# Kernel tuning notes

Measured on AMD Instinct MI355X. Metric: run time of the kernel, lower is better.

## Reference

```python
import jax, jax.numpy as jnp
import numpy as np

B = 8192      # rows after reshape(-1, seq_len)
S = 512       # seq_len
H = 256       # d_model (GRU hidden size)
P = 96        # pred_len
IN = 1        # GRUCell input size (scalar per step)


def setup_inputs() -> dict:
    key = jax.random.key(0)
    ks = jax.random.split(key, 7)
    s = 1.0 / np.sqrt(H)  # torch GRUCell init scale
    return {
        "x": jax.random.normal(ks[0], (B, S), dtype=jnp.float32),
        "W_ih": jax.random.uniform(ks[1], (3 * H, IN), jnp.float32, -s, s),
        "W_hh": jax.random.uniform(ks[2], (3 * H, H), jnp.float32, -s, s),
        "b_ih": jax.random.uniform(ks[3], (3 * H,), jnp.float32, -s, s),
        "b_hh": jax.random.uniform(ks[4], (3 * H,), jnp.float32, -s, s),
        "W_out": jax.random.uniform(ks[5], (P, H), jnp.float32, -s, s),
        "b_out": jax.random.uniform(ks[6], (P,), jnp.float32, -s, s),
    }


def reference(x, W_ih, W_hh, b_ih, b_hh, W_out, b_out):
    # Precompute input-side gate pre-activations for all timesteps at once:
    # x: [B, S], W_ih: [3H, 1] -> gi: [S, B, 3H]
    gi = x.T[:, :, None] * W_ih[:, 0][None, None, :] + b_ih  # [S, B, 3H]

    def step(h, gi_t):
        gh = h @ W_hh.T + b_hh                 # [B, 3H]
        i_r, i_z, i_n = jnp.split(gi_t, 3, axis=-1)
        h_r, h_z, h_n = jnp.split(gh, 3, axis=-1)
        r = jax.nn.sigmoid(i_r + h_r)
        z = jax.nn.sigmoid(i_z + h_z)
        n = jnp.tanh(i_n + r * h_n)
        h_new = (1.0 - z) * n + z * h
        return h_new, None

    h0 = jnp.zeros((x.shape[0], H), dtype=x.dtype)
    h_final, _ = jax.lax.scan(step, h0, gi)
    out = h_final @ W_out.T + b_out            # [B, P]
    return out.reshape(-1, P, 1)
```

## Files before the change

### kernel.cpp

```cpp
#include <hip/hip_runtime.h>
#include <math.h>

#define B_ROWS 8192
#define S_LEN  512
#define H_DIM  256
#define G3     768
#define P_DIM  96
#define TB     32

typedef __attribute__((ext_vector_type(8))) _Float16 half8;
typedef __attribute__((ext_vector_type(4))) float floatx4;

__device__ __forceinline__ float sigmoid_fast(float v) {
    return 1.0f / (1.0f + __expf(-v));
}
__device__ __forceinline__ float tanh_fast(float v) {
    return 1.0f - 2.0f / (__expf(2.0f * v) + 1.0f);
}
__device__ __forceinline__ unsigned short f32_f16(float f) {
    _Float16 h = (_Float16)f;
    return __builtin_bit_cast(unsigned short, h);
}
__device__ __forceinline__ int rot3(int l) { return ((l << 3) | (l >> 3)) & 63; }

__global__ void pack_weights(const float* __restrict__ W_hh,
                             const float* __restrict__ W_out,
                             unsigned short* __restrict__ Bh,
                             unsigned short* __restrict__ Bl,
                             float* __restrict__ WoT,
                             unsigned int* __restrict__ ctr) {
    const int j = blockIdx.x;
    const int k = threadIdx.x;
    const float wv = W_hh[j * H_DIM + k];
    const unsigned short hi = f32_f16(wv);
    const float hf = (float)__builtin_bit_cast(_Float16, hi);
    const unsigned short lo = f32_f16(wv - hf);
    const int idx = (((k >> 5) * 48 + (j >> 4)) * 64 +
                     ((j & 15) | (((k >> 3) & 3) << 4))) * 8 + (k & 7);
    Bh[idx] = hi;
    Bl[idx] = lo;
    if (j < P_DIM) WoT[k * P_DIM + j] = W_out[j * H_DIM + k];
    if (j == 0 && k == 0) *ctr = 0u;
}

#define A_OFF   0
#define X_OFF   32768
#define W_OFF   36864
#define LDS_SZ  135168

__device__ __forceinline__ void mfma2(floatx4& c0, floatx4& c1,
                                      const half8& a0, const half8& a1,
                                      const half8& bh, const half8& bl) {
    c0 = __builtin_amdgcn_mfma_f32_16x16x32_f16(a0, bh, c0, 0, 0, 0);
    c1 = __builtin_amdgcn_mfma_f32_16x16x32_f16(a1, bh, c1, 0, 0, 0);
    c0 = __builtin_amdgcn_mfma_f32_16x16x32_f16(a0, bl, c0, 0, 0, 0);
    c1 = __builtin_amdgcn_mfma_f32_16x16x32_f16(a1, bl, c1, 0, 0, 0);
}

__device__ __forceinline__ void gissue1(half8 (&BH)[6],
                                        const unsigned short* (&pbh)[6],
                                        int kc) {
#pragma unroll
    for (int gh = 0; gh < 6; ++gh)
        BH[gh] = *(const half8*)(pbh[gh] + (size_t)kc * 24576);
}

__device__ __forceinline__ void ahread(half8 (&AH)[2], const char* Ac,
                                       int kc, int rl) {
#pragma unroll
    for (int mt = 0; mt < 2; ++mt)
        AH[mt] = *(const half8*)(Ac + (kc * 2 + mt) * 1024 + rl * 16);
}

__device__ __forceinline__ void kcmfma1(floatx4 (&acc)[3][2][2],
                                        const half8 (&AH)[2],
                                        const half8 (&BH)[6]) {
#pragma unroll
    for (int gh = 0; gh < 6; ++gh) {
        floatx4& c0 = acc[gh >> 1][0][gh & 1];
        floatx4& c1 = acc[gh >> 1][1][gh & 1];
        c0 = __builtin_amdgcn_mfma_f32_16x16x32_f16(AH[0], BH[gh], c0, 0, 0, 0);
        c1 = __builtin_amdgcn_mfma_f32_16x16x32_f16(AH[1], BH[gh], c1, 0, 0, 0);
    }
}

__device__ __forceinline__ void kcmfma(floatx4 (&acc)[3][2][2],
                                       const half8 (&AH)[2],
                                       const half8 (&BH)[6],
                                       const half8 (&BL)[6]) {
#pragma unroll
    for (int gh = 0; gh < 6; ++gh)
        mfma2(acc[gh >> 1][0][gh & 1], acc[gh >> 1][1][gh & 1],
              AH[0], AH[1], BH[gh], BL[gh]);
}

__global__ __launch_bounds__(512, 2)
void gru_mfma(const float* __restrict__ x,
              const float* __restrict__ W_ih,
              const float* __restrict__ b_ih,
              const float* __restrict__ b_hh,
              const unsigned short* __restrict__ Bh,
              const unsigned short* __restrict__ Bl,
              const float* __restrict__ WoT,
              const float* __restrict__ b_out,
              float* __restrict__ out,
              unsigned int* __restrict__ ctr) {
    __shared__ __align__(16) char smem[LDS_SZ];

    const int tid  = threadIdx.x;
    const int w    = tid >> 6;
    const int lane = tid & 63;
    const int q    = lane >> 4;
    const int c    = lane & 15;
    const int row0 = blockIdx.x * TB;

    float wih[3][2], bcc[2][2], bihn[2], bhhn[2];
#pragma unroll
    for (int g = 0; g < 3; ++g)
#pragma unroll
        for (int ht = 0; ht < 2; ++ht) {
            const int col = g * H_DIM + w * 32 + ht * 16 + c;
            wih[g][ht] = W_ih[col];
            if (g < 2) {
                bcc[g][ht] = b_ih[col] + b_hh[col];
            } else {
                bihn[ht] = b_ih[col];
                bhhn[ht] = b_hh[col];
            }
        }

    const unsigned short* pbh[6];
    const unsigned short* pbl[6];
#pragma unroll
    for (int gh = 0; gh < 6; ++gh) {
        const size_t toff = (size_t)((gh >> 1) * 16 + w * 2 + (gh & 1)) * 512 + lane * 8;
        pbh[gh] = Bh + toff;
        pbl[gh] = Bl + toff;
    }

    half8 r7h[6], r7l[6];
#pragma unroll
    for (int gh = 0; gh < 6; ++gh) {
        r7h[gh] = *(const half8*)(pbh[gh] + 7 * 24576);
        r7l[gh] = *(const half8*)(pbl[gh] + 7 * 24576);
    }

    for (int i = tid; i < 96 * 64; i += 512) {
        const int slot = i >> 6, l16 = i & 63;
        const unsigned short* src = (slot < 48)
            ? (Bh + (size_t)(288 + slot) * 512 + l16 * 8)
            : (Bl + (size_t)(288 + slot - 48) * 512 + l16 * 8);
        *(uint4*)(smem + W_OFF + slot * 1024 + l16 * 16) = *(const uint4*)src;
    }

    for (int i = tid; i < 8192; i += 512) ((int*)(smem + A_OFF))[i] = 0;
    float* xt = (float*)(smem + X_OFF);
    {
        const int r = tid >> 4, t2 = tid & 15;
        xt[r * 16 + t2] = x[(size_t)(row0 + r) * S_LEN + t2];
    }
    __syncthreads();

    float h_own[2][2][4];
#pragma unroll
    for (int mt = 0; mt < 2; ++mt)
#pragma unroll
        for (int ht = 0; ht < 2; ++ht)
#pragma unroll
            for (int r = 0; r < 4; ++r) h_own[mt][ht][r] = 0.0f;

    const int rl = rot3(lane);

    int soff[2][4];
#pragma unroll
    for (int ht = 0; ht < 2; ++ht)
#pragma unroll
        for (int r = 0; r < 4; ++r) {
            const int d = (q * 4 + r) | ((2 * ht + (c >> 3)) << 4);
            soff[ht][r] = rot3(d) * 16 + (c & 7) * 2;
        }
    int xbase[2][4];
#pragma unroll
    for (int mt = 0; mt < 2; ++mt)
#pragma unroll
        for (int r = 0; r < 4; ++r)
            xbase[mt][r] = (q * 4 + r + 16 * mt) * 16;
    const char* w6base[6];
#pragma unroll
    for (int gh = 0; gh < 6; ++gh) {
        const int T = (gh >> 1) * 16 + w * 2 + (gh & 1);
        w6base[gh] = smem + W_OFF + T * 1024 + lane * 16;
    }

    half8 b0h[6], b1h[6];
    half8 ahA[2], ahB[2];

    gissue1(b0h, pbh, 0);

#pragma unroll 1
    for (int t = 0; t < S_LEN; ++t) {
#pragma unroll
        for (int gh = 0; gh < 6; ++gh)
            asm volatile("" : "+v"(pbh[gh]));

        const int cur = t & 1, nxt = cur ^ 1;
        const char* Ac = smem + A_OFF + cur * 16384;

        ahread(ahA, Ac, 0, rl);
        gissue1(b1h, pbh, 1);

        const int xidx = ((t >> 4) & 1) * 512 + (t & 15);
        float xr[2][4];
#pragma unroll
        for (int mt = 0; mt < 2; ++mt)
#pragma unroll
            for (int r = 0; r < 4; ++r)
                xr[mt][r] = xt[xbase[mt][r] + xidx];

        floatx4 acc[3][2][2];
#pragma unroll
        for (int mt = 0; mt < 2; ++mt)
#pragma unroll
            for (int ht = 0; ht < 2; ++ht)
#pragma unroll
                for (int r = 0; r < 4; ++r) {
                    acc[0][mt][ht][r] = fmaf(xr[mt][r], wih[0][ht], bcc[0][ht]);
                    acc[1][mt][ht][r] = fmaf(xr[mt][r], wih[1][ht], bcc[1][ht]);
                    acc[2][mt][ht][r] = bhhn[ht];
                }

        ahread(ahB, Ac, 1, rl);
        kcmfma1(acc, ahA, b0h);
        gissue1(b0h, pbh, 2);
        ahread(ahA, Ac, 2, rl);
        kcmfma1(acc, ahB, b1h);
        gissue1(b1h, pbh, 3);
        ahread(ahB, Ac, 3, rl);
        kcmfma1(acc, ahA, b0h);
        gissue1(b0h, pbh, 4);
        ahread(ahA, Ac, 4, rl);
        kcmfma1(acc, ahB, b1h);
        gissue1(b1h, pbh, 5);
        ahread(ahB, Ac, 5, rl);
        kcmfma1(acc, ahA, b0h);
        ahread(ahA, Ac, 6, rl);
        kcmfma1(acc, ahB, b1h);

        {
            half8 w6h[6], w6l[6];
#pragma unroll
            for (int gh = 0; gh < 6; ++gh) {
                w6h[gh] = *(const half8*)(w6base[gh]);
                w6l[gh] = *(const half8*)(w6base[gh] + 48 * 1024);
            }
            ahread(ahB, Ac, 7, rl);
            kcmfma(acc, ahA, w6h, w6l);
        }

        gissue1(b0h, pbh, 0);
        kcmfma(acc, ahB, r7h, r7l);

        char* Anx = smem + A_OFF + nxt * 16384;
#pragma unroll
        for (int mt = 0; mt < 2; ++mt) {
            char* ch = Anx + (w * 2 + mt) * 1024;
#pragma unroll
            for (int ht = 0; ht < 2; ++ht)
#pragma unroll
                for (int r = 0; r < 4; ++r) {
                    const float rr  = sigmoid_fast(acc[0][mt][ht][r]);
                    const float zz  = sigmoid_fast(acc[1][mt][ht][r]);
                    const float inn = fmaf(xr[mt][r], wih[2][ht], bihn[ht]);
                    const float nn  = tanh_fast(fmaf(rr, acc[2][mt][ht][r], inn));
                    const float hv  = (1.0f - zz) * nn + zz * h_own[mt][ht][r];
                    h_own[mt][ht][r] = hv;
                    *(unsigned short*)(ch + soff[ht][r]) = f32_f16(hv);
                }
        }

        const bool tick = ((t & 15) == 15) && (t != S_LEN - 1);
        if (tick) {
            const int r = tid >> 4, t2 = tid & 15;
            xt[((((t + 1) >> 4) & 1) * 32 + r) * 16 + t2] =
                x[(size_t)(row0 + r) * S_LEN + (t + 1) + t2];
        }
        __syncthreads();

        if (tick) {
            if (tid == 0) {
                const unsigned int tgt = 256u * (unsigned)((t >> 4) + 1);
                atomicAdd(ctr, 1u);
                for (int spin = 0; spin < (1 << 17); ++spin) {
                    if (__hip_atomic_load(ctr, __ATOMIC_RELAXED,
                                          __HIP_MEMORY_SCOPE_AGENT) >= tgt) break;
                    __builtin_amdgcn_s_sleep(4);
                }
            }
            __syncthreads();
        }
    }

    float* hfin = (float*)(smem);
#pragma unroll
    for (int mt = 0; mt < 2; ++mt)
#pragma unroll
        for (int ht = 0; ht < 2; ++ht)
#pragma unroll
            for (int r = 0; r < 4; ++r) {
                const int m = q * 4 + r + 16 * mt;
                const int k = w * 32 + ht * 16 + c;
                hfin[m * H_DIM + k] = h_own[mt][ht][r];
            }
    __syncthreads();

    if (tid < 256) {
        const int cid   = tid & 63;
        const int rid   = tid >> 6;
        const int myrow = rid * 8;
        const int pA    = cid;
        const int pB    = 64 + cid;
        const bool hasB = (cid < 32);
        float accA[8], accB[8];
#pragma unroll
        for (int rr = 0; rr < 8; ++rr) { accA[rr] = 0.0f; accB[rr] = 0.0f; }

        for (int k = 0; k < H_DIM; k += 4) {
            float4 hv[8];
#pragma unroll
            for (int rr = 0; rr < 8; ++rr)
                hv[rr] = *(const float4*)&hfin[(myrow + rr) * H_DIM + k];
            float wA[4], wB[4];
#pragma unroll
            for (int kk = 0; kk < 4; ++kk) {
                wA[kk] = WoT[(size_t)(k + kk) * P_DIM + pA];
                wB[kk] = hasB ? WoT[(size_t)(k + kk) * P_DIM + pB] : 0.0f;
            }
#pragma unroll
            for (int kk = 0; kk < 4; ++kk)
#pragma unroll
                for (int rr = 0; rr < 8; ++rr) {
                    const float hvv = (&hv[rr].x)[kk];
                    accA[rr] = fmaf(hvv, wA[kk], accA[rr]);
                    accB[rr] = fmaf(hvv, wB[kk], accB[rr]);
                }
        }
        const float boA = b_out[pA];
        const float boB = hasB ? b_out[pB] : 0.0f;
#pragma unroll
        for (int rr = 0; rr < 8; ++rr) {
            const size_t orow = (size_t)(row0 + myrow + rr) * P_DIM;
            out[orow + pA] = accA[rr] + boA;
            if (hasB) out[orow + pB] = accB[rr] + boB;
        }
    }
}

__global__ __launch_bounds__(256, 1)
void gru_fallback(const float* __restrict__ x,
                  const float* __restrict__ W_ih,
                  const float* __restrict__ Whh,
                  const float* __restrict__ b_ih,
                  const float* __restrict__ b_hh,
                  const float* __restrict__ Wout,
                  const float* __restrict__ b_out,
                  float* __restrict__ out) {
    __shared__ float hbuf[2][TB][H_DIM];

    const int tid   = threadIdx.x;
    const int cid   = tid & 63;
    const int rid   = tid >> 6;
    const int row0  = blockIdx.x * TB;
    const int myrow = rid * 8;
    const int c0    = cid * 4;

    float wih[3][4], bc[2][4], bihn[4], bhhn[4];
#pragma unroll
    for (int cc = 0; cc < 4; ++cc) {
        const int j = c0 + cc;
        wih[0][cc] = W_ih[j];
        wih[1][cc] = W_ih[H_DIM + j];
        wih[2][cc] = W_ih[2 * H_DIM + j];
        bc[0][cc]  = b_ih[j] + b_hh[j];
        bc[1][cc]  = b_ih[H_DIM + j] + b_hh[H_DIM + j];
        bihn[cc]   = b_ih[2 * H_DIM + j];
        bhhn[cc]   = b_hh[2 * H_DIM + j];
    }
    for (int i = tid; i < TB * H_DIM; i += 256) (&hbuf[0][0][0])[i] = 0.0f;
    float h_own[8][4];
#pragma unroll
    for (int rr = 0; rr < 8; ++rr)
#pragma unroll
        for (int cc = 0; cc < 4; ++cc) h_own[rr][cc] = 0.0f;
    __syncthreads();

    int p = 0;
    for (int t = 0; t < S_LEN; ++t) {
        float xv[8];
#pragma unroll
        for (int rr = 0; rr < 8; ++rr)
            xv[rr] = x[(size_t)(row0 + myrow + rr) * S_LEN + t];

        float acc[3][8][4];
#pragma unroll
        for (int rr = 0; rr < 8; ++rr)
#pragma unroll
            for (int cc = 0; cc < 4; ++cc) {
                acc[0][rr][cc] = fmaf(xv[rr], wih[0][cc], bc[0][cc]);
                acc[1][rr][cc] = fmaf(xv[rr], wih[1][cc], bc[1][cc]);
                acc[2][rr][cc] = bhhn[cc];
            }
        const float* hb = &hbuf[p][0][0];
        for (int k = 0; k < H_DIM; k += 4) {
            float4 hv[8];
#pragma unroll
            for (int rr = 0; rr < 8; ++rr)
                hv[rr] = *(const float4*)(hb + (myrow + rr) * H_DIM + k);
#pragma unroll
            for (int g = 0; g < 3; ++g)
#pragma unroll
                for (int kk = 0; kk < 4; ++kk) {
                    float wrow[4];
#pragma unroll
                    for (int cc = 0; cc < 4; ++cc)
                        wrow[cc] = Whh[(size_t)(g * H_DIM + c0 + cc) * H_DIM + k + kk];
#pragma unroll
                    for (int rr = 0; rr < 8; ++rr) {
                        const float hvv = (&hv[rr].x)[kk];
#pragma unroll
                        for (int cc = 0; cc < 4; ++cc)
                            acc[g][rr][cc] = fmaf(hvv, wrow[cc], acc[g][rr][cc]);
                    }
                }
        }
#pragma unroll
        for (int rr = 0; rr < 8; ++rr) {
            float4 hnew;
#pragma unroll
            for (int cc = 0; cc < 4; ++cc) {
                const float r_  = sigmoid_fast(acc[0][rr][cc]);
                const float z_  = sigmoid_fast(acc[1][rr][cc]);
                const float i_n = fmaf(xv[rr], wih[2][cc], bihn[cc]);
                const float n_  = tanh_fast(fmaf(r_, acc[2][rr][cc], i_n));
                const float hv2 = (1.0f - z_) * n_ + z_ * h_own[rr][cc];
                h_own[rr][cc] = hv2;
                (&hnew.x)[cc] = hv2;
            }
            *(float4*)&hbuf[1 - p][myrow + rr][c0] = hnew;
        }
        __syncthreads();
        p ^= 1;
    }

    const int  pA   = cid;
    const int  pB   = 64 + cid;
    const bool hasB = (cid < 32);
    float accA[8], accB[8];
#pragma unroll
    for (int rr = 0; rr < 8; ++rr) { accA[rr] = 0.0f; accB[rr] = 0.0f; }
    for (int k = 0; k < H_DIM; k += 4) {
        float4 hv[8];
#pragma unroll
        for (int rr = 0; rr < 8; ++rr)
            hv[rr] = *(const float4*)&hbuf[p][myrow + rr][k];
        float wA[4], wB[4];
#pragma unroll
        for (int kk = 0; kk < 4; ++kk) {
            wA[kk] = Wout[(size_t)pA * H_DIM + k + kk];
            wB[kk] = hasB ? Wout[(size_t)pB * H_DIM + k + kk] : 0.0f;
        }
#pragma unroll
        for (int kk = 0; kk < 4; ++kk)
#pragma unroll
            for (int rr = 0; rr < 8; ++rr) {
                const float hvv = (&hv[rr].x)[kk];
                accA[rr] = fmaf(hvv, wA[kk], accA[rr]);
                accB[rr] = fmaf(hvv, wB[kk], accB[rr]);
            }
    }
    const float boA = b_out[pA];
    const float boB = hasB ? b_out[pB] : 0.0f;
#pragma unroll
    for (int rr = 0; rr < 8; ++rr) {
        const size_t orow = (size_t)(row0 + myrow + rr) * P_DIM;
        out[orow + pA] = accA[rr] + boA;
        if (hasB) out[orow + pB] = accB[rr] + boB;
    }
}

extern "C" void kernel_launch(void* const* d_in, const int* in_sizes, int n_in,
                              void* d_out, int out_size, void* d_ws, size_t ws_size,
                              hipStream_t stream) {
    const float* x     = (const float*)d_in[0];
    const float* W_ih  = (const float*)d_in[1];
    const float* W_hh  = (const float*)d_in[2];
    const float* b_ih  = (const float*)d_in[3];
    const float* b_hh  = (const float*)d_in[4];
    const float* W_out = (const float*)d_in[5];
    const float* b_out = (const float*)d_in[6];
    float* out = (float*)d_out;

    const size_t bpack_elems = 8 * 48 * 64 * 8;
    const size_t wot_elems   = (size_t)H_DIM * P_DIM;
    const size_t ctr_off = bpack_elems * 2 * sizeof(unsigned short) * 2 +
                           wot_elems * sizeof(float);
    const size_t need = ctr_off + sizeof(unsigned int);

    if (ws_size >= need) {
        unsigned short* Bh = (unsigned short*)d_ws;
        unsigned short* Bl = Bh + bpack_elems * 2;
        float* WoT = (float*)(Bl + bpack_elems * 2);
        unsigned int* ctr = (unsigned int*)((char*)d_ws + ctr_off);
        pack_weights<<<G3, H_DIM, 0, stream>>>(W_hh, W_out, Bh, Bl, WoT, ctr);
        gru_mfma<<<B_ROWS / TB, 512, 0, stream>>>(x, W_ih, b_ih, b_hh,
                                                  Bh, Bl, WoT, b_out, out, ctr);
    } else {
        gru_fallback<<<B_ROWS / TB, 256, 0, stream>>>(x, W_ih, W_hh, b_ih, b_hh,
                                                      W_out, b_out, out);
    }
}
```

Measured before the change: 3.485 ms.

## Halve rows per GRU block to double resident blocks per CU

Each block now handles 16 batch rows instead of 32, with one M tile per wave. Launch bounds ask for four blocks per SM, and the grid barrier target is updated for 512 blocks. The low half of the fp16-split weights for k-chunk 6 is dropped from LDS, so only chunk 7 keeps the hi+lo correction. The aim is more waves per CU to hide MFMA and load latency and a smaller LDS footprint. The cost is twice the per-CU streaming of W_hh from L2 per step, tighter register limits, and slightly lower precision.

```diff
diff --git a/kernel.cpp b/kernel.cpp
--- a/kernel.cpp
+++ b/kernel.cpp
@@ -6,7 +6,7 @@
 #define H_DIM  256
 #define G3     768
 #define P_DIM  96
-#define TB     32
+#define TB     16
 
 typedef __attribute__((ext_vector_type(8))) _Float16 half8;
 typedef __attribute__((ext_vector_type(4))) float floatx4;
@@ -44,18 +44,9 @@
 }
 
 #define A_OFF   0
-#define X_OFF   32768
-#define W_OFF   36864
-#define LDS_SZ  135168
-
-__device__ __forceinline__ void mfma2(floatx4& c0, floatx4& c1,
-                                      const half8& a0, const half8& a1,
-                                      const half8& bh, const half8& bl) {
-    c0 = __builtin_amdgcn_mfma_f32_16x16x32_f16(a0, bh, c0, 0, 0, 0);
-    c1 = __builtin_amdgcn_mfma_f32_16x16x32_f16(a1, bh, c1, 0, 0, 0);
-    c0 = __builtin_amdgcn_mfma_f32_16x16x32_f16(a0, bl, c0, 0, 0, 0);
-    c1 = __builtin_amdgcn_mfma_f32_16x16x32_f16(a1, bl, c1, 0, 0, 0);
-}
+#define X_OFF   16384
+#define W_OFF   18432
+#define LDS_SZ  67584
 
 __device__ __forceinline__ void gissue1(half8 (&BH)[6],
                                         const unsigned short* (&pbh)[6],
@@ -65,36 +56,34 @@
         BH[gh] = *(const half8*)(pbh[gh] + (size_t)kc * 24576);
 }
 
-__device__ __forceinline__ void ahread(half8 (&AH)[2], const char* Ac,
-                                       int kc, int rl) {
-#pragma unroll
-    for (int mt = 0; mt < 2; ++mt)
-        AH[mt] = *(const half8*)(Ac + (kc * 2 + mt) * 1024 + rl * 16);
-}
-
-__device__ __forceinline__ void kcmfma1(floatx4 (&acc)[3][2][2],
-                                        const half8 (&AH)[2],
+__device__ __forceinline__ void ahread1(half8& AH, const char* Ac,
+                                        int kc, int rl) {
+    AH = *(const half8*)(Ac + kc * 1024 + rl * 16);
+}
+
+__device__ __forceinline__ void kcmfma1(floatx4 (&acc)[3][2],
+                                        const half8& AH,
                                         const half8 (&BH)[6]) {
 #pragma unroll
     for (int gh = 0; gh < 6; ++gh) {
-        floatx4& c0 = acc[gh >> 1][0][gh & 1];
-        floatx4& c1 = acc[gh >> 1][1][gh & 1];
-        c0 = __builtin_amdgcn_mfma_f32_16x16x32_f16(AH[0], BH[gh], c0, 0, 0, 0);
-        c1 = __builtin_amdgcn_mfma_f32_16x16x32_f16(AH[1], BH[gh], c1, 0, 0, 0);
-    }
-}
-
-__device__ __forceinline__ void kcmfma(floatx4 (&acc)[3][2][2],
-                                       const half8 (&AH)[2],
-                                       const half8 (&BH)[6],
-                                       const half8 (&BL)[6]) {
-#pragma unroll
-    for (int gh = 0; gh < 6; ++gh)
-        mfma2(acc[gh >> 1][0][gh & 1], acc[gh >> 1][1][gh & 1],
-              AH[0], AH[1], BH[gh], BL[gh]);
-}
-
-__global__ __launch_bounds__(512, 2)
+        floatx4& c = acc[gh >> 1][gh & 1];
+        c = __builtin_amdgcn_mfma_f32_16x16x32_f16(AH, BH[gh], c, 0, 0, 0);
+    }
+}
+
+__device__ __forceinline__ void kcmfma2(floatx4 (&acc)[3][2],
+                                        const half8& AH,
+                                        const half8 (&BH)[6],
+                                        const half8 (&BL)[6]) {
+#pragma unroll
+    for (int gh = 0; gh < 6; ++gh) {
+        floatx4& c = acc[gh >> 1][gh & 1];
+        c = __builtin_amdgcn_mfma_f32_16x16x32_f16(AH, BH[gh], c, 0, 0, 0);
+        c = __builtin_amdgcn_mfma_f32_16x16x32_f16(AH, BL[gh], c, 0, 0, 0);
+    }
+}
+
+__global__ __launch_bounds__(512, 4)
 void gru_mfma(const float* __restrict__ x,
               const float* __restrict__ W_ih,
               const float* __restrict__ b_ih,
@@ -145,29 +134,25 @@
         r7l[gh] = *(const half8*)(pbl[gh] + 7 * 24576);
     }
 
-    for (int i = tid; i < 96 * 64; i += 512) {
+    for (int i = tid; i < 48 * 64; i += 512) {
         const int slot = i >> 6, l16 = i & 63;
-        const unsigned short* src = (slot < 48)
-            ? (Bh + (size_t)(288 + slot) * 512 + l16 * 8)
-            : (Bl + (size_t)(288 + slot - 48) * 512 + l16 * 8);
+        const unsigned short* src = Bh + (size_t)(288 + slot) * 512 + l16 * 8;
         *(uint4*)(smem + W_OFF + slot * 1024 + l16 * 16) = *(const uint4*)src;
     }
 
-    for (int i = tid; i < 8192; i += 512) ((int*)(smem + A_OFF))[i] = 0;
+    for (int i = tid; i < 4096; i += 512) ((int*)(smem + A_OFF))[i] = 0;
     float* xt = (float*)(smem + X_OFF);
-    {
+    if (tid < 256) {
         const int r = tid >> 4, t2 = tid & 15;
         xt[r * 16 + t2] = x[(size_t)(row0 + r) * S_LEN + t2];
     }
     __syncthreads();
 
-    float h_own[2][2][4];
-#pragma unroll
-    for (int mt = 0; mt < 2; ++mt)
-#pragma unroll
-        for (int ht = 0; ht < 2; ++ht)
-#pragma unroll
-            for (int r = 0; r < 4; ++r) h_own[mt][ht][r] = 0.0f;
+    float h_own[2][4];
+#pragma unroll
+    for (int ht = 0; ht < 2; ++ht)
+#pragma unroll
+        for (int r = 0; r < 4; ++r) h_own[ht][r] = 0.0f;
 
     const int rl = rot3(lane);
 
@@ -179,12 +164,9 @@
             const int d = (q * 4 + r) | ((2 * ht + (c >> 3)) << 4);
             soff[ht][r] = rot3(d) * 16 + (c & 7) * 2;
         }
-    int xbase[2][4];
-#pragma unroll
-    for (int mt = 0; mt < 2; ++mt)
-#pragma unroll
-        for (int r = 0; r < 4; ++r)
-            xbase[mt][r] = (q * 4 + r + 16 * mt) * 16;
+    int xbase[4];
+#pragma unroll
+    for (int r = 0; r < 4; ++r) xbase[r] = (q * 4 + r) * 16;
     const char* w6base[6];
 #pragma unroll
     for (int gh = 0; gh < 6; ++gh) {
@@ -193,7 +175,7 @@
     }
 
     half8 b0h[6], b1h[6];
-    half8 ahA[2], ahB[2];
+    half8 ahA, ahB;
 
     gissue1(b0h, pbh, 0);
 
@@ -204,91 +186,81 @@
             asm volatile("" : "+v"(pbh[gh]));
 
         const int cur = t & 1, nxt = cur ^ 1;
-        const char* Ac = smem + A_OFF + cur * 16384;
-
-        ahread(ahA, Ac, 0, rl);
+        const char* Ac = smem + A_OFF + cur * 8192;
+
+        ahread1(ahA, Ac, 0, rl);
         gissue1(b1h, pbh, 1);
 
-        const int xidx = ((t >> 4) & 1) * 512 + (t & 15);
-        float xr[2][4];
-#pragma unroll
-        for (int mt = 0; mt < 2; ++mt)
-#pragma unroll
-            for (int r = 0; r < 4; ++r)
-                xr[mt][r] = xt[xbase[mt][r] + xidx];
-
-        floatx4 acc[3][2][2];
-#pragma unroll
-        for (int mt = 0; mt < 2; ++mt)
-#pragma unroll
-            for (int ht = 0; ht < 2; ++ht)
-#pragma unroll
-                for (int r = 0; r < 4; ++r) {
-                    acc[0][mt][ht][r] = fmaf(xr[mt][r], wih[0][ht], bcc[0][ht]);
-                    acc[1][mt][ht][r] = fmaf(xr[mt][r], wih[1][ht], bcc[1][ht]);
-                    acc[2][mt][ht][r] = bhhn[ht];
-                }
-
-        ahread(ahB, Ac, 1, rl);
+        const int xidx = ((t >> 4) & 1) * 256 + (t & 15);
+        float xr[4];
+#pragma unroll
+        for (int r = 0; r < 4; ++r) xr[r] = xt[xbase[r] + xidx];
+
+        floatx4 acc[3][2];
+#pragma unroll
+        for (int ht = 0; ht < 2; ++ht)
+#pragma unroll
+            for (int r = 0; r < 4; ++r) {
+                acc[0][ht][r] = fmaf(xr[r], wih[0][ht], bcc[0][ht]);
+                acc[1][ht][r] = fmaf(xr[r], wih[1][ht], bcc[1][ht]);
+                acc[2][ht][r] = bhhn[ht];
+            }
+
+        ahread1(ahB, Ac, 1, rl);
         kcmfma1(acc, ahA, b0h);
         gissue1(b0h, pbh, 2);
-        ahread(ahA, Ac, 2, rl);
+        ahread1(ahA, Ac, 2, rl);
         kcmfma1(acc, ahB, b1h);
         gissue1(b1h, pbh, 3);
-        ahread(ahB, Ac, 3, rl);
+        ahread1(ahB, Ac, 3, rl);
         kcmfma1(acc, ahA, b0h);
         gissue1(b0h, pbh, 4);
-        ahread(ahA, Ac, 4, rl);
+        ahread1(ahA, Ac, 4, rl);
         kcmfma1(acc, ahB, b1h);
         gissue1(b1h, pbh, 5);
-        ahread(ahB, Ac, 5, rl);
+        ahread1(ahB, Ac, 5, rl);
         kcmfma1(acc, ahA, b0h);
-        ahread(ahA, Ac, 6, rl);
+        ahread1(ahA, Ac, 6, rl);
         kcmfma1(acc, ahB, b1h);
 
         {
-            half8 w6h[6], w6l[6];
-#pragma unroll
-            for (int gh = 0; gh < 6; ++gh) {
+            half8 w6h[6];
+#pragma unroll
+            for (int gh = 0; gh < 6; ++gh)
                 w6h[gh] = *(const half8*)(w6base[gh]);
-                w6l[gh] = *(const half8*)(w6base[gh] + 48 * 1024);
-            }
-            ahread(ahB, Ac, 7, rl);
-            kcmfma(acc, ahA, w6h, w6l);
+            ahread1(ahB, Ac, 7, rl);
+            kcmfma1(acc, ahA, w6h);
         }
 
         gissue1(b0h, pbh, 0);
-        kcmfma(acc, ahB, r7h, r7l);
-
-        char* Anx = smem + A_OFF + nxt * 16384;
-#pragma unroll
-        for (int mt = 0; mt < 2; ++mt) {
-            char* ch = Anx + (w * 2 + mt) * 1024;
-#pragma unroll
-            for (int ht = 0; ht < 2; ++ht)
-#pragma unroll
-                for (int r = 0; r < 4; ++r) {
-                    const float rr  = sigmoid_fast(acc[0][mt][ht][r]);
-                    const float zz  = sigmoid_fast(acc[1][mt][ht][r]);
-                    const float inn = fmaf(xr[mt][r], wih[2][ht], bihn[ht]);
-                    const float nn  = tanh_fast(fmaf(rr, acc[2][mt][ht][r], inn));
-                    const float hv  = (1.0f - zz) * nn + zz * h_own[mt][ht][r];
-                    h_own[mt][ht][r] = hv;
-                    *(unsigned short*)(ch + soff[ht][r]) = f32_f16(hv);
-                }
-        }
+        kcmfma2(acc, ahB, r7h, r7l);
+
+        char* Anx = smem + A_OFF + nxt * 8192;
+        char* ch  = Anx + w * 1024;
+#pragma unroll
+        for (int ht = 0; ht < 2; ++ht)
+#pragma unroll
+            for (int r = 0; r < 4; ++r) {
+                const float rr  = sigmoid_fast(acc[0][ht][r]);
+                const float zz  = sigmoid_fast(acc[1][ht][r]);
+                const float inn = fmaf(xr[r], wih[2][ht], bihn[ht]);
+                const float nn  = tanh_fast(fmaf(rr, acc[2][ht][r], inn));
+                const float hv  = (1.0f - zz) * nn + zz * h_own[ht][r];
+                h_own[ht][r] = hv;
+                *(unsigned short*)(ch + soff[ht][r]) = f32_f16(hv);
+            }
 
         const bool tick = ((t & 15) == 15) && (t != S_LEN - 1);
-        if (tick) {
+        if (tick && tid < 256) {
             const int r = tid >> 4, t2 = tid & 15;
-            xt[((((t + 1) >> 4) & 1) * 32 + r) * 16 + t2] =
+            xt[((((t + 1) >> 4) & 1) * 16 + r) * 16 + t2] =
                 x[(size_t)(row0 + r) * S_LEN + (t + 1) + t2];
         }
         __syncthreads();
 
         if (tick) {
             if (tid == 0) {
-                const unsigned int tgt = 256u * (unsigned)((t >> 4) + 1);
+                const unsigned int tgt = 512u * (unsigned)((t >> 4) + 1);
                 atomicAdd(ctr, 1u);
                 for (int spin = 0; spin < (1 << 17); ++spin) {
                     if (__hip_atomic_load(ctr, __ATOMIC_RELAXED,
@@ -302,32 +274,30 @@
 
     float* hfin = (float*)(smem);
 #pragma unroll
-    for (int mt = 0; mt < 2; ++mt)
-#pragma unroll
-        for (int ht = 0; ht < 2; ++ht)
-#pragma unroll
-            for (int r = 0; r < 4; ++r) {
-                const int m = q * 4 + r + 16 * mt;
-                const int k = w * 32 + ht * 16 + c;
-                hfin[m * H_DIM + k] = h_own[mt][ht][r];
-            }
+    for (int ht = 0; ht < 2; ++ht)
+#pragma unroll
+        for (int r = 0; r < 4; ++r) {
+            const int m = q * 4 + r;
+            const int k = w * 32 + ht * 16 + c;
+            hfin[m * H_DIM + k] = h_own[ht][r];
+        }
     __syncthreads();
 
     if (tid < 256) {
         const int cid   = tid & 63;
         const int rid   = tid >> 6;
-        const int myrow = rid * 8;
+        const int myrow = rid * 4;
         const int pA    = cid;
         const int pB    = 64 + cid;
         const bool hasB = (cid < 32);
-        float accA[8], accB[8];
-#pragma unroll
-        for (int rr = 0; rr < 8; ++rr) { accA[rr] = 0.0f; accB[rr] = 0.0f; }
+        float accA[4], accB[4];
+#pragma unroll
+        for (int rr = 0; rr < 4; ++rr) { accA[rr] = 0.0f; accB[rr] = 0.0f; }
 
         for (int k = 0; k < H_DIM; k += 4) {
-            float4 hv[8];
-#pragma unroll
-            for (int rr = 0; rr < 8; ++rr)
+            float4 hv[4];
+#pragma unroll
+            for (int rr = 0; rr < 4; ++rr)
                 hv[rr] = *(const float4*)&hfin[(myrow + rr) * H_DIM + k];
             float wA[4], wB[4];
 #pragma unroll
@@ -338,7 +308,7 @@
 #pragma unroll
             for (int kk = 0; kk < 4; ++kk)
 #pragma unroll
-                for (int rr = 0; rr < 8; ++rr) {
+                for (int rr = 0; rr < 4; ++rr) {
                     const float hvv = (&hv[rr].x)[kk];
                     accA[rr] = fmaf(hvv, wA[kk], accA[rr]);
                     accB[rr] = fmaf(hvv, wB[kk], accB[rr]);
@@ -347,7 +317,7 @@
         const float boA = b_out[pA];
         const float boB = hasB ? b_out[pB] : 0.0f;
 #pragma unroll
-        for (int rr = 0; rr < 8; ++rr) {
+        for (int rr = 0; rr < 4; ++rr) {
             const size_t orow = (size_t)(row0 + myrow + rr) * P_DIM;
             out[orow + pA] = accA[rr] + boA;
             if (hasB) out[orow + pB] = accB[rr] + boB;
@@ -355,6 +325,7 @@
     }
 }
 
+#define FTB 32
 __global__ __launch_bounds__(256, 1)
 void gru_fallback(const float* __restrict__ x,
                   const float* __restrict__ W_ih,
@@ -364,12 +335,12 @@
                   const float* __restrict__ Wout,
                   const float* __restrict__ b_out,
                   float* __restrict__ out) {
-    __shared__ float hbuf[2][TB][H_DIM];
+    __shared__ float hbuf[2][FTB][H_DIM];
 
     const int tid   = threadIdx.x;
     const int cid   = tid & 63;
     const int rid   = tid >> 6;
-    const int row0  = blockIdx.x * TB;
+    const int row0  = blockIdx.x * FTB;
     const int myrow = rid * 8;
     const int c0    = cid * 4;
 
@@ -385,7 +356,7 @@
         bihn[cc]   = b_ih[2 * H_DIM + j];
         bhhn[cc]   = b_hh[2 * H_DIM + j];
     }
-    for (int i = tid; i < TB * H_DIM; i += 256) (&hbuf[0][0][0])[i] = 0.0f;
+    for (int i = tid; i < FTB * H_DIM; i += 256) (&hbuf[0][0][0])[i] = 0.0f;
     float h_own[8][4];
 #pragma unroll
     for (int rr = 0; rr < 8; ++rr)
@@ -514,7 +485,7 @@
         gru_mfma<<<B_ROWS / TB, 512, 0, stream>>>(x, W_ih, b_ih, b_hh,
                                                   Bh, Bl, WoT, b_out, out, ctr);
     } else {
-        gru_fallback<<<B_ROWS / TB, 256, 0, stream>>>(x, W_ih, W_hh, b_ih, b_hh,
+        gru_fallback<<<B_ROWS / 32, 256, 0, stream>>>(x, W_ih, W_hh, b_ih, b_hh,
                                                       W_out, b_out, out);
     }
 }
```

New measurement: 8.188 ms. +135.0%, slower.
